# Performance work log

Hardware: AMD Instinct MI355X
Metric: run time of the kernel (lower is better)

## Reference

```python
import jax, jax.numpy as jnp
import numpy as np

R = 524288   # rays (batch_ray scaled to production)
NC = 64      # num_coarse
NF = 128     # num_fine
NEAR, FAR = 2.0, 6.0


def setup_inputs() -> dict:
    key = jax.random.key(0)
    k1, = jax.random.split(key, 1)
    # sigma from a Sigmoid head -> (0, 1)
    sigma_coarse = jax.random.uniform(k1, (R, NC), dtype=jnp.float32)
    # t_coarse = linspace(near, far, num_coarse) per ray, as in render_rays
    t_coarse = jnp.broadcast_to(jnp.linspace(NEAR, FAR, NC, dtype=jnp.float32), (R, NC))
    return {"t_coarse": t_coarse, "sigma_coarse": sigma_coarse}


def reference(t_coarse, sigma_coarse):
    """Vectorized NeRF hierarchical inverse-CDF resampling.

    Per ray (original resample(), loop-free):
      cdf = cumsum(sigma); t_inv = interior linspace(cdf[0], cdf[-1], NF+2)
      idx = last j with cdf[j] < t_inv[i]   (== searchsorted(left) - 1)
      t_fine = t_coarse[idx] + (t_inv - cdf[idx]) * delta / sigma[idx+1]
    """
    cdf = jnp.cumsum(sigma_coarse, axis=1)                      # [R, NC]
    low = cdf[:, :1]                                            # min(cdf) (sigma > 0)
    high = cdf[:, -1:]                                          # max(cdf)
    delta = t_coarse[:, 1:2] - t_coarse[:, 0:1]                 # uniform spacing
    slope_inv = delta / sigma_coarse[:, 1:]                     # [R, NC-1]

    nf = NF
    frac = (jnp.arange(1, nf + 1, dtype=jnp.float32) / (nf + 1))[None, :]
    t_inv = low + (high - low) * frac                           # [R, NF] interior points

    # last index where cdf < t_inv  (strict t_inv > cdf as in original)
    idx = jax.vmap(lambda c, t: jnp.searchsorted(c, t, side='left'))(cdf, t_inv) - 1
    idx = jnp.clip(idx, 0, NC - 2)                              # valid for slope_inv too

    t0 = jnp.take_along_axis(t_coarse, idx, axis=1)
    c0 = jnp.take_along_axis(cdf, idx, axis=1)
    si = jnp.take_along_axis(slope_inv, idx, axis=1)
    t_fine = t0 + (t_inv - c0) * si                             # [R, NF]
    return t_fine
```

## Files before the change

### kernel.cpp

```cpp
#include <hip/hip_runtime.h>


constexpr int NC = 64;
constexpr int NF = 128;
constexpr int RPW = 4;
constexpr int WPB = 4;
constexpr int BLOCK = WPB * 64;
constexpr int RPB = WPB * RPW;

typedef float f32x4 __attribute__((ext_vector_type(4)));

template <int CTRL, bool BOUND>
__device__ __forceinline__ int dpp_mov_i(int x) {
    return __builtin_amdgcn_update_dpp(0, x, CTRL, 0xF, 0xF, BOUND);
}
template <int CTRL, bool BOUND>
__device__ __forceinline__ float dpp_mov_f(float x) {
    return __builtin_bit_cast(float,
        dpp_mov_i<CTRL, BOUND>(__builtin_bit_cast(int, x)));
}

__global__ __launch_bounds__(BLOCK) void nerf_resample_kernel(
    const float* __restrict__ t_coarse,
    const float* __restrict__ sigma_coarse,
    float* __restrict__ out,
    int n_rays)
{
    __shared__ alignas(16) float2 ab[WPB][RPW][NF];

    const int lane = threadIdx.x & 63;
    const int wave = threadIdx.x >> 6;
    const int g    = lane >> 4;
    const int q    = lane & 15;

    int ray = blockIdx.x * RPB + wave * RPW + g;
    if (ray >= n_rays) ray = n_rays - 1;

    const size_t base = (size_t)ray * NC;

    const float4 v  = *(const float4*)(sigma_coarse + base + 4 * q);
    const float2 tp = *(const float2*)(t_coarse + base);
    const float t0 = tp.x;
    const float dt = tp.y - tp.x;

    const float p0 = v.x;
    const float p1 = p0 + v.y;
    const float p2 = p1 + v.z;
    const float p3 = p2 + v.w;

    float S = p3;
    S += dpp_mov_f<0x111, false>(S);
    S += dpp_mov_f<0x112, false>(S);
    S += dpp_mov_f<0x114, false>(S);
    S += dpp_mov_f<0x118, false>(S);
    const float E = S - p3;

    const float c0 = E + p0;
    const float c1 = E + p1;
    const float c2 = E + p2;
    const float c3 = E + p3;

    const int rowbase = lane & 48;
    const float low  = __shfl(c0, rowbase, 64);
    const float high = __shfl(c3, rowbase + 15, 64);
    const float span = high - low;
    const float kf = 129.0f * __builtin_amdgcn_rcpf(span);

    int M0 = (int)((c0 - low) * kf);
    int M1 = (int)((c1 - low) * kf);
    int M2 = (int)((c2 - low) * kf);
    int M3 = (int)((c3 - low) * kf);
    M0 = min(M0, NF); M1 = min(M1, NF); M2 = min(M2, NF); M3 = min(M3, NF);
    int   M4 = dpp_mov_i<0x101, true>(M0);
    float sn = dpp_mov_f<0x101, true>(v.x);
    if (q == 15) M4 = NF;

    const float B0 = dt * __builtin_amdgcn_rcpf(v.y);
    const float B1 = dt * __builtin_amdgcn_rcpf(v.z);
    const float B2 = dt * __builtin_amdgcn_rcpf(v.w);
    const float B3 = dt * __builtin_amdgcn_rcpf(sn);
    const int jb = 4 * q;
    auto pack = [](float B, int j) -> float {
        unsigned b = __builtin_bit_cast(unsigned, B);
        return __builtin_bit_cast(float, (b & ~63u) | (unsigned)j);
    };
    const float2 sl0 = make_float2(c0, pack(B0, jb + 0));
    const float2 sl1 = make_float2(c1, pack(B1, jb + 1));
    const float2 sl2 = make_float2(c2, pack(B2, jb + 2));
    const float2 sl3 = make_float2(c3, pack(B3, jb + 3));

    float2* myb = ab[wave][g];
    for (int i = M0; i < M1; ++i) myb[i] = sl0;
    for (int i = M1; i < M2; ++i) myb[i] = sl1;
    for (int i = M2; i < M3; ++i) myb[i] = sl2;
    for (int i = M3; i < M4; ++i) myb[i] = sl3;

    constexpr float u1 = 1.0f / 129.0f;
    const int ray0 = blockIdx.x * RPB + wave * RPW;
    const int half = lane >> 5;
    const int q2   = lane & 31;
    const int i0   = 4 * q2;

    #pragma unroll
    for (int p = 0; p < 2; ++p) {
        const int rr   = 2 * p + half;
        const int srcl = 16 * rr;
        const float lo_r = __shfl(low,  srcl, 64);
        const float sp_r = __shfl(span, srcl, 64);
        const float t0_r = __shfl(t0,   srcl, 64);
        const float dt_r = __shfl(dt,   srcl, 64);
        int ray_r = ray0 + rr;
        if (ray_r >= n_rays) ray_r = n_rays - 1;

        const float4 sa = *(const float4*)&ab[wave][rr][i0];
        const float4 sb = *(const float4*)&ab[wave][rr][i0 + 2];

        const float tinv0 = fmaf(sp_r, (float)(i0 + 1) * u1, lo_r);
        const float tinv1 = fmaf(sp_r, (float)(i0 + 2) * u1, lo_r);
        const float tinv2 = fmaf(sp_r, (float)(i0 + 3) * u1, lo_r);
        const float tinv3 = fmaf(sp_r, (float)(i0 + 4) * u1, lo_r);

        const int j0 = (int)(__builtin_bit_cast(unsigned, sa.y) & 63u);
        const int j1 = (int)(__builtin_bit_cast(unsigned, sa.w) & 63u);
        const int j2 = (int)(__builtin_bit_cast(unsigned, sb.y) & 63u);
        const int j3 = (int)(__builtin_bit_cast(unsigned, sb.w) & 63u);

        const float r0 = fmaf(tinv0 - sa.x, sa.y, fmaf((float)j0, dt_r, t0_r));
        const float r1 = fmaf(tinv1 - sa.z, sa.w, fmaf((float)j1, dt_r, t0_r));
        const float r2 = fmaf(tinv2 - sb.x, sb.y, fmaf((float)j2, dt_r, t0_r));
        const float r3 = fmaf(tinv3 - sb.z, sb.w, fmaf((float)j3, dt_r, t0_r));

        f32x4 rv = { r0, r1, r2, r3 };
        __builtin_nontemporal_store(rv,
            (f32x4*)(out + (size_t)ray_r * NF + i0));
    }
}

extern "C" void kernel_launch(void* const* d_in, const int* in_sizes, int n_in,
                              void* d_out, int out_size, void* d_ws, size_t ws_size,
                              hipStream_t stream) {
    const float* t_coarse     = (const float*)d_in[0];
    const float* sigma_coarse = (const float*)d_in[1];
    float* out = (float*)d_out;

    const int n_rays = in_sizes[0] / NC;
    const int blocks = (n_rays + RPB - 1) / RPB;

    nerf_resample_kernel<<<blocks, BLOCK, 0, stream>>>(
        t_coarse, sigma_coarse, out, n_rays);
}
```

Baseline: 71.62 us.

## Use persistent grid-stride blocks with next-group prefetch and affine-folded segment coefficients

The kernel now launches a fixed grid of 2048 blocks. Each block loops over ray groups with a grid stride and loads the next group's sigma and t values before computing the current group, so global loads overlap with compute. It also folds the per-segment math into an affine form (intercept, slope per fine index) stored in LDS, so the output phase is a single FMA per element and no longer needs shuffles or index unpacking. The costs are a loop-carried register footprint, no sync between iterations that reuse the same LDS row, and possible small rounding differences from the refactored arithmetic.

```diff
diff --git a/kernel.cpp b/kernel.cpp
--- a/kernel.cpp
+++ b/kernel.cpp
@@ -7,6 +7,7 @@
 constexpr int WPB = 4;
 constexpr int BLOCK = WPB * 64;
 constexpr int RPB = WPB * RPW;
+constexpr int GRID = 2048;
 
 typedef float f32x4 __attribute__((ext_vector_type(4)));
 
@@ -33,106 +34,115 @@
     const int g    = lane >> 4;
     const int q    = lane & 15;
 
-    int ray = blockIdx.x * RPB + wave * RPW + g;
-    if (ray >= n_rays) ray = n_rays - 1;
+    const int n_groups = (n_rays + RPB - 1) / RPB;
 
-    const size_t base = (size_t)ray * NC;
-
-    const float4 v  = *(const float4*)(sigma_coarse + base + 4 * q);
-    const float2 tp = *(const float2*)(t_coarse + base);
-    const float t0 = tp.x;
-    const float dt = tp.y - tp.x;
-
-    const float p0 = v.x;
-    const float p1 = p0 + v.y;
-    const float p2 = p1 + v.z;
-    const float p3 = p2 + v.w;
-
-    float S = p3;
-    S += dpp_mov_f<0x111, false>(S);
-    S += dpp_mov_f<0x112, false>(S);
-    S += dpp_mov_f<0x114, false>(S);
-    S += dpp_mov_f<0x118, false>(S);
-    const float E = S - p3;
-
-    const float c0 = E + p0;
-    const float c1 = E + p1;
-    const float c2 = E + p2;
-    const float c3 = E + p3;
-
-    const int rowbase = lane & 48;
-    const float low  = __shfl(c0, rowbase, 64);
-    const float high = __shfl(c3, rowbase + 15, 64);
-    const float span = high - low;
-    const float kf = 129.0f * __builtin_amdgcn_rcpf(span);
-
-    int M0 = (int)((c0 - low) * kf);
-    int M1 = (int)((c1 - low) * kf);
-    int M2 = (int)((c2 - low) * kf);
-    int M3 = (int)((c3 - low) * kf);
-    M0 = min(M0, NF); M1 = min(M1, NF); M2 = min(M2, NF); M3 = min(M3, NF);
-    int   M4 = dpp_mov_i<0x101, true>(M0);
-    float sn = dpp_mov_f<0x101, true>(v.x);
-    if (q == 15) M4 = NF;
-
-    const float B0 = dt * __builtin_amdgcn_rcpf(v.y);
-    const float B1 = dt * __builtin_amdgcn_rcpf(v.z);
-    const float B2 = dt * __builtin_amdgcn_rcpf(v.w);
-    const float B3 = dt * __builtin_amdgcn_rcpf(sn);
-    const int jb = 4 * q;
-    auto pack = [](float B, int j) -> float {
-        unsigned b = __builtin_bit_cast(unsigned, B);
-        return __builtin_bit_cast(float, (b & ~63u) | (unsigned)j);
-    };
-    const float2 sl0 = make_float2(c0, pack(B0, jb + 0));
-    const float2 sl1 = make_float2(c1, pack(B1, jb + 1));
-    const float2 sl2 = make_float2(c2, pack(B2, jb + 2));
-    const float2 sl3 = make_float2(c3, pack(B3, jb + 3));
-
-    float2* myb = ab[wave][g];
-    for (int i = M0; i < M1; ++i) myb[i] = sl0;
-    for (int i = M1; i < M2; ++i) myb[i] = sl1;
-    for (int i = M2; i < M3; ++i) myb[i] = sl2;
-    for (int i = M3; i < M4; ++i) myb[i] = sl3;
-
-    constexpr float u1 = 1.0f / 129.0f;
-    const int ray0 = blockIdx.x * RPB + wave * RPW;
     const int half = lane >> 5;
     const int q2   = lane & 31;
     const int i0   = 4 * q2;
+    const float f0 = (float)(i0 + 1);
+    const float f1 = f0 + 1.0f;
+    const float f2 = f0 + 2.0f;
+    const float f3 = f0 + 3.0f;
 
-    #pragma unroll
-    for (int p = 0; p < 2; ++p) {
-        const int rr   = 2 * p + half;
-        const int srcl = 16 * rr;
-        const float lo_r = __shfl(low,  srcl, 64);
-        const float sp_r = __shfl(span, srcl, 64);
-        const float t0_r = __shfl(t0,   srcl, 64);
-        const float dt_r = __shfl(dt,   srcl, 64);
-        int ray_r = ray0 + rr;
-        if (ray_r >= n_rays) ray_r = n_rays - 1;
+    int grp = blockIdx.x;
+    if (grp >= n_groups) return;
 
-        const float4 sa = *(const float4*)&ab[wave][rr][i0];
-        const float4 sb = *(const float4*)&ab[wave][rr][i0 + 2];
+    auto ray_of = [&](int gg) {
+        int r = gg * RPB + wave * RPW + g;
+        return r < n_rays ? r : n_rays - 1;
+    };
 
-        const float tinv0 = fmaf(sp_r, (float)(i0 + 1) * u1, lo_r);
-        const float tinv1 = fmaf(sp_r, (float)(i0 + 2) * u1, lo_r);
-        const float tinv2 = fmaf(sp_r, (float)(i0 + 3) * u1, lo_r);
-        const float tinv3 = fmaf(sp_r, (float)(i0 + 4) * u1, lo_r);
+    size_t base = (size_t)ray_of(grp) * NC;
+    float4 v  = *(const float4*)(sigma_coarse + base + 4 * q);
+    float2 tp = *(const float2*)(t_coarse + base);
 
-        const int j0 = (int)(__builtin_bit_cast(unsigned, sa.y) & 63u);
-        const int j1 = (int)(__builtin_bit_cast(unsigned, sa.w) & 63u);
-        const int j2 = (int)(__builtin_bit_cast(unsigned, sb.y) & 63u);
-        const int j3 = (int)(__builtin_bit_cast(unsigned, sb.w) & 63u);
+    while (true) {
+        const int gnext = grp + GRID;
+        const bool last = gnext >= n_groups;
+        const size_t nbase = (size_t)ray_of(last ? grp : gnext) * NC;
+        const float4 vn  = *(const float4*)(sigma_coarse + nbase + 4 * q);
+        const float2 tpn = *(const float2*)(t_coarse + nbase);
 
-        const float r0 = fmaf(tinv0 - sa.x, sa.y, fmaf((float)j0, dt_r, t0_r));
-        const float r1 = fmaf(tinv1 - sa.z, sa.w, fmaf((float)j1, dt_r, t0_r));
-        const float r2 = fmaf(tinv2 - sb.x, sb.y, fmaf((float)j2, dt_r, t0_r));
-        const float r3 = fmaf(tinv3 - sb.z, sb.w, fmaf((float)j3, dt_r, t0_r));
+        const float t0 = tp.x;
+        const float dt = tp.y - tp.x;
 
-        f32x4 rv = { r0, r1, r2, r3 };
-        __builtin_nontemporal_store(rv,
-            (f32x4*)(out + (size_t)ray_r * NF + i0));
+        const float p0 = v.x;
+        const float p1 = p0 + v.y;
+        const float p2 = p1 + v.z;
+        const float p3 = p2 + v.w;
+
+        float S = p3;
+        S += dpp_mov_f<0x111, false>(S);
+        S += dpp_mov_f<0x112, false>(S);
+        S += dpp_mov_f<0x114, false>(S);
+        S += dpp_mov_f<0x118, false>(S);
+        const float E = S - p3;
+
+        const float c0 = E + p0;
+        const float c1 = E + p1;
+        const float c2 = E + p2;
+        const float c3 = E + p3;
+
+        const int rowbase = lane & 48;
+        const float low  = __shfl(c0, rowbase, 64);
+        const float high = __shfl(c3, rowbase + 15, 64);
+        const float span = high - low;
+        const float kf   = 129.0f * __builtin_amdgcn_rcpf(span);
+        const float sp_u = span * (1.0f / 129.0f);
+
+        const float e0 = c0 - low;
+        const float e1 = c1 - low;
+        const float e2 = c2 - low;
+        const float e3 = c3 - low;
+        int M0 = (int)(e0 * kf);
+        int M1 = (int)(e1 * kf);
+        int M2 = (int)(e2 * kf);
+        int M3 = (int)(e3 * kf);
+        M0 = min(M0, NF); M1 = min(M1, NF); M2 = min(M2, NF); M3 = min(M3, NF);
+        int   M4 = dpp_mov_i<0x101, true>(M0);
+        float sn = dpp_mov_f<0x101, true>(v.x);
+        if (q == 15) M4 = NF;
+
+        const float B0 = dt * __builtin_amdgcn_rcpf(v.y);
+        const float B1 = dt * __builtin_amdgcn_rcpf(v.z);
+        const float B2 = dt * __builtin_amdgcn_rcpf(v.w);
+        const float B3 = dt * __builtin_amdgcn_rcpf(sn);
+        const int jb = 4 * q;
+        const float tj0 = fmaf((float)jb, dt, t0);
+        const float tj1 = tj0 + dt;
+        const float tj2 = tj1 + dt;
+        const float tj3 = tj2 + dt;
+        const float2 sl0 = make_float2(fmaf(-e0, B0, tj0), sp_u * B0);
+        const float2 sl1 = make_float2(fmaf(-e1, B1, tj1), sp_u * B1);
+        const float2 sl2 = make_float2(fmaf(-e2, B2, tj2), sp_u * B2);
+        const float2 sl3 = make_float2(fmaf(-e3, B3, tj3), sp_u * B3);
+
+        float2* myb = ab[wave][g];
+        for (int i = M0; i < M1; ++i) myb[i] = sl0;
+        for (int i = M1; i < M2; ++i) myb[i] = sl1;
+        for (int i = M2; i < M3; ++i) myb[i] = sl2;
+        for (int i = M3; i < M4; ++i) myb[i] = sl3;
+
+        const int ray0 = grp * RPB + wave * RPW;
+        #pragma unroll
+        for (int p = 0; p < 2; ++p) {
+            const int rr = 2 * p + half;
+            int ray_r = ray0 + rr;
+            if (ray_r >= n_rays) ray_r = n_rays - 1;
+
+            const float4 sa = *(const float4*)&ab[wave][rr][i0];
+            const float4 sb = *(const float4*)&ab[wave][rr][i0 + 2];
+
+            f32x4 rv = { fmaf(f0, sa.y, sa.x),
+                         fmaf(f1, sa.w, sa.z),
+                         fmaf(f2, sb.y, sb.x),
+                         fmaf(f3, sb.w, sb.z) };
+            __builtin_nontemporal_store(rv,
+                (f32x4*)(out + (size_t)ray_r * NF + i0));
+        }
+
+        if (last) break;
+        v = vn; tp = tpn; grp = gnext;
     }
 }
 
@@ -143,8 +153,9 @@
     const float* sigma_coarse = (const float*)d_in[1];
     float* out = (float*)d_out;
 
-    const int n_rays = in_sizes[0] / NC;
-    const int blocks = (n_rays + RPB - 1) / RPB;
+    const int n_rays   = in_sizes[0] / NC;
+    const int n_groups = (n_rays + RPB - 1) / RPB;
+    const int blocks   = n_groups < GRID ? n_groups : GRID;
 
     nerf_resample_kernel<<<blocks, BLOCK, 0, stream>>>(
         t_coarse, sigma_coarse, out, n_rays);
```

Measured after the change: 77.73 us. +8.5%, slower.
